# Kernel tuning notes

Hardware: AMD Instinct MI355X
Metric: run time of the kernel (lower is better)

Reference implementation:

```python
import jax, jax.numpy as jnp
import numpy as np

IN_FEATURES = 512
OUT_FEATURES = 256
N = 2048

def setup_inputs() -> dict:
    key = jax.random.key(0)
    k1, k2, k3 = jax.random.split(key, 3)
    x = jax.random.normal(k1, (N, IN_FEATURES), dtype=jnp.float32)
    # kaiming_uniform_(a=sqrt(5)) -> uniform(-b, b) with b = sqrt(6/((1+5)*fan_in)) = 1/sqrt(fan_in)
    bound_w = 1.0 / np.sqrt(IN_FEATURES)
    weight = jax.random.uniform(k2, (OUT_FEATURES, IN_FEATURES), dtype=jnp.float32,
                                minval=-bound_w, maxval=bound_w)
    bound_b = 1.0 / np.sqrt(IN_FEATURES)
    bias = jax.random.uniform(k3, (OUT_FEATURES,), dtype=jnp.float32,
                              minval=-bound_b, maxval=bound_b)
    return {"x": x, "weight": weight, "bias": bias}

def reference(x, weight, bias):
    # MAM fully-connected (beta == 0 path):
    # prod[n, k, j] = x[n, k] * weight[j, k]
    # C[n, j] = max_k prod[n,k,j] + min_k prod[n,k,j] + bias[j]
    prod = x[:, :, None] * weight.T[None, :, :]   # [N, in, out]
    C = jnp.max(prod, axis=1) + jnp.min(prod, axis=1) + bias[None, :]
    return C
```

## Files before the change

kernel.cpp:

```cpp
#include <hip/hip_runtime.h>
#include <math.h>

#define N_ 2048
#define K_ 512
#define J_ 256
#define TN 64
#define TJ 32
#define BK 256
#define RP 260

typedef __attribute__((address_space(3))) float       lds_f;
typedef const __attribute__((address_space(1))) float glb_f;

__global__ __launch_bounds__(256) void mam_fused(
    const float* __restrict__ x, const float* __restrict__ w,
    const float* __restrict__ bias, float* __restrict__ out)
{
    __shared__ __align__(16) float xs[TN * RP];
    __shared__ __align__(16) float wsh[TJ * RP];

    const int t    = threadIdx.x;
    const int lane = t & 63;
    const int wid  = t >> 6;
    const int j0   = blockIdx.x * TJ;
    const int n0   = blockIdx.y * TN;
    const int tx   = t & 15;
    const int ty   = t >> 4;

    float mx[4][2], mn[4][2];
#pragma unroll
    for (int i = 0; i < 4; ++i)
#pragma unroll
        for (int j = 0; j < 2; ++j) {
            mx[i][j] = -__builtin_inff();
            mn[i][j] =  __builtin_inff();
        }

    for (int kc = 0; kc < K_; kc += BK) {
#pragma unroll
        for (int r = 0; r < 16; ++r) {
            const int row = wid * 16 + r;
            __builtin_amdgcn_global_load_lds(
                (glb_f*)(x + (size_t)(n0 + row) * K_ + kc + lane * 4),
                (lds_f*)(xs + row * RP), 16, 0, 0);
        }
#pragma unroll
        for (int r = 0; r < 8; ++r) {
            const int row = wid * 8 + r;
            __builtin_amdgcn_global_load_lds(
                (glb_f*)(w + (size_t)(j0 + row) * K_ + kc + lane * 4),
                (lds_f*)(wsh + row * RP), 16, 0, 0);
        }
        __syncthreads();

#pragma unroll 4
        for (int kk = 0; kk < BK; kk += 4) {
            float4 xv[4], wq[2];
#pragma unroll
            for (int i = 0; i < 4; ++i)
                xv[i] = *(const float4*)&xs[(ty * 4 + i) * RP + kk];
#pragma unroll
            for (int j = 0; j < 2; ++j)
                wq[j] = *(const float4*)&wsh[(tx * 2 + j) * RP + kk];
#pragma unroll
            for (int i = 0; i < 4; ++i) {
                const float xa[4] = {xv[i].x, xv[i].y, xv[i].z, xv[i].w};
#pragma unroll
                for (int j = 0; j < 2; ++j) {
                    const float wa[4] = {wq[j].x, wq[j].y, wq[j].z, wq[j].w};
#pragma unroll
                    for (int q = 0; q < 4; ++q) {
                        const float p = xa[q] * wa[q];
                        mx[i][j] = fmaxf(mx[i][j], p);
                        mn[i][j] = fminf(mn[i][j], p);
                    }
                }
            }
        }
        __syncthreads();
    }

    const float2 bi = *(const float2*)&bias[j0 + tx * 2];
#pragma unroll
    for (int i = 0; i < 4; ++i) {
        float2 o;
        o.x = mx[i][0] + mn[i][0] + bi.x;
        o.y = mx[i][1] + mn[i][1] + bi.y;
        *(float2*)&out[(size_t)(n0 + ty * 4 + i) * J_ + j0 + tx * 2] = o;
    }
}

extern "C" void kernel_launch(void* const* d_in, const int* in_sizes, int n_in,
                              void* d_out, int out_size, void* d_ws, size_t ws_size,
                              hipStream_t stream) {
    const float* x    = (const float*)d_in[0];
    const float* w    = (const float*)d_in[1];
    const float* bias = (const float*)d_in[2];
    float* out = (float*)d_out;

    dim3 grid(J_ / TJ, N_ / TN);
    mam_fused<<<grid, 256, 0, stream>>>(x, w, bias, out);
}
```

Before: 82.94 us.

## Stage full x tile in swizzled LDS and stream wave-uniform weights as scalar loads

The kernel now loads the whole 64-row x tile (all of K) into LDS once, using an XOR-swizzled k-major layout, and drops the per-chunk global_load_lds path along with its second barrier. Each wave owns 8 output columns. Because the weight addresses are wave-uniform, weight rows are read straight from global memory, where the compiler can turn them into scalar loads instead of staging them in LDS. Each lane handles one row, keeps 8 max/min pairs, and writes float4 outputs. In exchange, x reuse per thread drops, weights are re-read per block from cache, the kernel uses 128 KB of LDS, which limits occupancy to one block per CU, and the grid order is swapped.

```diff
diff --git a/kernel.cpp b/kernel.cpp
--- a/kernel.cpp
+++ b/kernel.cpp
@@ -4,90 +4,61 @@
 #define N_ 2048
 #define K_ 512
 #define J_ 256
-#define TN 64
-#define TJ 32
-#define BK 256
-#define RP 260
-
-typedef __attribute__((address_space(3))) float       lds_f;
-typedef const __attribute__((address_space(1))) float glb_f;
+#define BN 64
+#define BJ 32
+#define K4 (K_ / 4)
 
 __global__ __launch_bounds__(256) void mam_fused(
     const float* __restrict__ x, const float* __restrict__ w,
     const float* __restrict__ bias, float* __restrict__ out)
 {
-    __shared__ __align__(16) float xs[TN * RP];
-    __shared__ __align__(16) float wsh[TJ * RP];
+    __shared__ __align__(16) float4 xs[K4 * BN];
 
     const int t    = threadIdx.x;
     const int lane = t & 63;
-    const int wid  = t >> 6;
-    const int j0   = blockIdx.x * TJ;
-    const int n0   = blockIdx.y * TN;
-    const int tx   = t & 15;
-    const int ty   = t >> 4;
+    const int widx = __builtin_amdgcn_readfirstlane(t >> 6);
+    const int n0    = blockIdx.x * BN;
+    const int jbase = blockIdx.y * BJ + widx * 8;
 
-    float mx[4][2], mn[4][2];
+    float mx[8], mn[8];
 #pragma unroll
-    for (int i = 0; i < 4; ++i)
+    for (int j = 0; j < 8; ++j) { mx[j] = -__builtin_inff(); mn[j] = __builtin_inff(); }
+
 #pragma unroll
-        for (int j = 0; j < 2; ++j) {
-            mx[i][j] = -__builtin_inff();
-            mn[i][j] =  __builtin_inff();
+    for (int r = 0; r < 32; ++r) {
+        const int idx = r * 256 + t;
+        const int nn  = idx >> 7;
+        const int k4  = idx & (K4 - 1);
+        const float4 g = *(const float4*)(x + (size_t)(n0 + nn) * K_ + k4 * 4);
+        xs[k4 * BN + (nn ^ (k4 & 63))] = g;
+    }
+    __syncthreads();
+
+    const float* wc = w + (size_t)jbase * K_;
+#pragma unroll 2
+    for (int k4 = 0; k4 < K4; ++k4) {
+        const float4 xv = xs[k4 * BN + (lane ^ (k4 & 63))];
+#pragma unroll
+        for (int jj = 0; jj < 8; ++jj) {
+            const float4 wv = *(const float4*)(wc + jj * K_ + k4 * 4);
+            const float p0 = xv.x * wv.x;
+            const float p1 = xv.y * wv.y;
+            const float p2 = xv.z * wv.z;
+            const float p3 = xv.w * wv.w;
+            mx[jj] = fmaxf(fmaxf(mx[jj], p0), p1);
+            mn[jj] = fminf(fminf(mn[jj], p0), p1);
+            mx[jj] = fmaxf(fmaxf(mx[jj], p2), p3);
+            mn[jj] = fminf(fminf(mn[jj], p2), p3);
         }
-
-    for (int kc = 0; kc < K_; kc += BK) {
-#pragma unroll
-        for (int r = 0; r < 16; ++r) {
-            const int row = wid * 16 + r;
-            __builtin_amdgcn_global_load_lds(
-                (glb_f*)(x + (size_t)(n0 + row) * K_ + kc + lane * 4),
-                (lds_f*)(xs + row * RP), 16, 0, 0);
-        }
-#pragma unroll
-        for (int r = 0; r < 8; ++r) {
-            const int row = wid * 8 + r;
-            __builtin_amdgcn_global_load_lds(
-                (glb_f*)(w + (size_t)(j0 + row) * K_ + kc + lane * 4),
-                (lds_f*)(wsh + row * RP), 16, 0, 0);
-        }
-        __syncthreads();
-
-#pragma unroll 4
-        for (int kk = 0; kk < BK; kk += 4) {
-            float4 xv[4], wq[2];
-#pragma unroll
-            for (int i = 0; i < 4; ++i)
-                xv[i] = *(const float4*)&xs[(ty * 4 + i) * RP + kk];
-#pragma unroll
-            for (int j = 0; j < 2; ++j)
-                wq[j] = *(const float4*)&wsh[(tx * 2 + j) * RP + kk];
-#pragma unroll
-            for (int i = 0; i < 4; ++i) {
-                const float xa[4] = {xv[i].x, xv[i].y, xv[i].z, xv[i].w};
-#pragma unroll
-                for (int j = 0; j < 2; ++j) {
-                    const float wa[4] = {wq[j].x, wq[j].y, wq[j].z, wq[j].w};
-#pragma unroll
-                    for (int q = 0; q < 4; ++q) {
-                        const float p = xa[q] * wa[q];
-                        mx[i][j] = fmaxf(mx[i][j], p);
-                        mn[i][j] = fminf(mn[i][j], p);
-                    }
-                }
-            }
-        }
-        __syncthreads();
     }
 
-    const float2 bi = *(const float2*)&bias[j0 + tx * 2];
+    const float* bb = bias + jbase;
+    float o[8];
 #pragma unroll
-    for (int i = 0; i < 4; ++i) {
-        float2 o;
-        o.x = mx[i][0] + mn[i][0] + bi.x;
-        o.y = mx[i][1] + mn[i][1] + bi.y;
-        *(float2*)&out[(size_t)(n0 + ty * 4 + i) * J_ + j0 + tx * 2] = o;
-    }
+    for (int jj = 0; jj < 8; ++jj) o[jj] = mx[jj] + mn[jj] + bb[jj];
+    float* op = out + (size_t)(n0 + lane) * J_ + jbase;
+    *(float4*)(op)     = make_float4(o[0], o[1], o[2], o[3]);
+    *(float4*)(op + 4) = make_float4(o[4], o[5], o[6], o[7]);
 }
 
 extern "C" void kernel_launch(void* const* d_in, const int* in_sizes, int n_in,
@@ -98,6 +69,6 @@
     const float* bias = (const float*)d_in[2];
     float* out = (float*)d_out;
 
-    dim3 grid(J_ / TJ, N_ / TN);
+    dim3 grid(N_ / BN, J_ / BJ);
     mam_fused<<<grid, 256, 0, stream>>>(x, w, bias, out);
 }
```

Result: slower. 99.65 us (+20.1%).
